# Performance work log

Measured on AMD Instinct MI355X. Metric: run time of the kernel, lower is better.

## Reference

```python
import jax, jax.numpy as jnp
import numpy as np

N_ATOMS = 100000
N_BONDS = 400000
ATOM_FDIM = 133
BOND_FDIM = 147
HIDDEN = 300
DEPTH = 3


def setup_inputs() -> dict:
    key = jax.random.key(0)
    ks = jax.random.split(key, 10)
    f_atoms = jax.random.normal(ks[0], (N_ATOMS, ATOM_FDIM), dtype=jnp.float32)
    f_bonds = jax.random.normal(ks[1], (N_BONDS, BOND_FDIM), dtype=jnp.float32)
    b2a = jax.random.randint(ks[2], (N_BONDS,), 0, N_ATOMS)
    b2revb = jax.random.randint(ks[3], (N_BONDS,), 0, N_BONDS)
    s_i = 1.0 / np.sqrt(BOND_FDIM)
    s_h = 1.0 / np.sqrt(HIDDEN)
    s_o = 1.0 / np.sqrt(ATOM_FDIM + HIDDEN)
    Wi_w = jax.random.uniform(ks[4], (HIDDEN, BOND_FDIM), jnp.float32, -s_i, s_i)
    Wi_b = jax.random.uniform(ks[5], (HIDDEN,), jnp.float32, -s_i, s_i)
    Wh_w = jax.random.uniform(ks[6], (HIDDEN, HIDDEN), jnp.float32, -s_h, s_h)
    Wh_b = jax.random.uniform(ks[7], (HIDDEN,), jnp.float32, -s_h, s_h)
    Wo_w = jax.random.uniform(ks[8], (HIDDEN, ATOM_FDIM + HIDDEN), jnp.float32, -s_o, s_o)
    Wo_b = jax.random.uniform(ks[9], (HIDDEN,), jnp.float32, -s_o, s_o)
    return {"f_atoms": f_atoms, "f_bonds": f_bonds, "b2a": b2a, "b2revb": b2revb,
            "Wi_w": Wi_w, "Wi_b": Wi_b, "Wh_w": Wh_w, "Wh_b": Wh_b,
            "Wo_w": Wo_w, "Wo_b": Wo_b}


def reference(f_atoms, f_bonds, b2a, b2revb, Wi_w, Wi_b, Wh_w, Wh_b, Wo_w, Wo_b):
    n_atoms = f_atoms.shape[0]
    # initial bond messages: [n_bonds, hidden]
    H_bonds = jax.nn.relu(f_bonds @ Wi_w.T + Wi_b)
    dest = b2a[b2revb]  # destination atom of each directed bond
    for _ in range(DEPTH - 1):
        # scatter-add bond messages onto destination atoms
        sum_msgs = jax.ops.segment_sum(H_bonds, dest, num_segments=n_atoms)
        # gather back to bonds from source atoms, subtract reverse-bond message
        msgs = sum_msgs[b2a] - H_bonds[b2revb]
        H_bonds = jax.nn.relu(H_bonds + msgs @ Wh_w.T + Wh_b)
    sum_msgs = jax.ops.segment_sum(H_bonds, dest, num_segments=n_atoms)
    H_atoms = jax.nn.relu(jnp.concatenate([f_atoms, sum_msgs], axis=1) @ Wo_w.T + Wo_b)
    return (H_atoms, H_bonds)
```

## Files before the change

kernel.cpp:

```cpp
#include <hip/hip_runtime.h>
#include <hip/hip_bf16.h>

#define NB 400000
#define NA 100000
#define AFD 133
#define BFD 147
#define HID 300
#define NP  320
#define SMP 304
#define NT  98

typedef short short8 __attribute__((ext_vector_type(8)));
typedef float f32x4 __attribute__((ext_vector_type(4)));

__device__ __forceinline__ ushort f2b(float f) {
    union { float f; unsigned u; } v; v.f = f;
    unsigned r = v.u + 0x7fffu + ((v.u >> 16) & 1u);
    return (ushort)(r >> 16);
}
__device__ __forceinline__ float b2f(ushort u) {
    union { unsigned u; float f; } v; v.u = ((unsigned)u) << 16;
    return v.f;
}

#define GLDS(gp, lp) __builtin_amdgcn_global_load_lds( \
    (const __attribute__((address_space(1))) void*)(gp), \
    (__attribute__((address_space(3))) void*)(lp), 16, 0, 0)


__global__ void pad_w_k(const float* __restrict__ W, ushort* __restrict__ Wp,
                        int N, int K, int Kp) {
    int idx = blockIdx.x * 256 + threadIdx.x;
    if (idx >= NP * Kp) return;
    int n = idx / Kp, k = idx - n * Kp;
    int t = k >> 5, kk = k & 31;
    int g = kk >> 3, s = kk & 7;
    int gp = g ^ ((n >> 1) & 3);
    ushort v = (n < N && k < K) ? f2b(W[n * K + k]) : (ushort)0;
    Wp[(size_t)t * 10240 + n * 32 + gp * 8 + s] = v;
}

__global__ void pad_bias_k(const float* __restrict__ bh, float* __restrict__ bhp) {
    int i = blockIdx.x * 256 + threadIdx.x;
    if (i < NP) bhp[i] = (i < HID) ? bh[i] : 0.f;
}

__global__ void dest_k(const int* __restrict__ b2a, const int* __restrict__ b2revb,
                       int* __restrict__ dest) {
    int b = blockIdx.x * 256 + threadIdx.x;
    if (b < NB) dest[b] = b2a[b2revb[b]];
}

__global__ void count_k(const int* __restrict__ dest, int* __restrict__ cnt) {
    int b = blockIdx.x * 256 + threadIdx.x;
    if (b < NB) atomicAdd(&cnt[dest[b]], 1);
}

__global__ void scanA_k(const int* __restrict__ cnt, int* __restrict__ tsum) {
    __shared__ int sm[256];
    const int tid = threadIdx.x;
    int base = blockIdx.x * 1024 + tid * 4;
    int s = 0;
#pragma unroll
    for (int j = 0; j < 4; ++j) { int i = base + j; if (i < NA) s += cnt[i]; }
    sm[tid] = s; __syncthreads();
    for (int o = 128; o > 0; o >>= 1) {
        if (tid < o) sm[tid] += sm[tid + o];
        __syncthreads();
    }
    if (tid == 0) tsum[blockIdx.x] = sm[0];
}

__global__ void scanB_k(const int* __restrict__ tsum, int* __restrict__ toff,
                        int* __restrict__ rs) {
    if (threadIdx.x == 0) {
        int run = 0;
        for (int t = 0; t < NT; ++t) { toff[t] = run; run += tsum[t]; }
        rs[NA] = run;
    }
}

__global__ void scanC_k(const int* __restrict__ cnt, const int* __restrict__ toff,
                        int* __restrict__ rs) {
    __shared__ int sm[256];
    const int tid = threadIdx.x;
    int base = blockIdx.x * 1024 + tid * 4;
    int v[4]; int s = 0;
#pragma unroll
    for (int j = 0; j < 4; ++j) {
        v[j] = (base + j < NA) ? cnt[base + j] : 0;
        s += v[j];
    }
    sm[tid] = s; __syncthreads();
    for (int o = 1; o < 256; o <<= 1) {
        int x = (tid >= o) ? sm[tid - o] : 0;
        __syncthreads();
        sm[tid] += x;
        __syncthreads();
    }
    int acc = sm[tid] - s + toff[blockIdx.x];
#pragma unroll
    for (int j = 0; j < 4; ++j) {
        if (base + j < NA) rs[base + j] = acc;
        acc += v[j];
    }
}

__global__ void scatter_k(const int* __restrict__ dest, const int* __restrict__ rs,
                          int* __restrict__ cur, int* __restrict__ bl) {
    int b = blockIdx.x * 256 + threadIdx.x;
    if (b >= NB) return;
    int a = dest[b];
    int pos = rs[a] + atomicAdd(&cur[a], 1);
    bl[pos] = b;
}

template<int MODE>
__global__ __launch_bounds__(512) void gemm_k(
    const float* __restrict__ F1, const float* __restrict__ Sum,
    const ushort* __restrict__ W, const float* __restrict__ bias,
    ushort* __restrict__ Cb, float* __restrict__ Cf, int M)
{
    constexpr int KP = (MODE == 0) ? 192 : 448;
    constexpr int TILES = KP / 32;
    static_assert(KP % 64 == 0 && TILES % 2 == 0, "XOR swizzle needs 128B rows, even tiles");
    __shared__ ushort As[128 * KP];
    __shared__ ushort Bs[2][320 * 32];

    const int tid = threadIdx.x;
    const int w = tid >> 6, lane = tid & 63;
    const int wr = w >> 2, wc = w & 3;
    const int g = lane >> 4, lr = lane & 15;
    const int m0 = blockIdx.x * 128;

    {
        const int row = tid >> 2, q = tid & 3;
        int grow = m0 + row;
        if (MODE == 2 && grow >= M) grow = M - 1;
        const int axw = (row & 7) << 4;
        char* abase = (char*)As + (size_t)row * (KP * 2);
#pragma unroll
        for (int t = 0; t < TILES; ++t) {
            const int k0 = t * 32 + q * 8;
            ushort o[8];
            if (MODE == 0) {
                const float* src = F1 + (size_t)grow * BFD;
#pragma unroll
                for (int s = 0; s < 8; ++s)
                    o[s] = (k0 + s < BFD) ? f2b(src[k0 + s]) : (ushort)0;
            } else {
#pragma unroll
                for (int s = 0; s < 8; ++s) {
                    int k = k0 + s;
                    float x = 0.f;
                    if (k < AFD) x = F1[(size_t)grow * AFD + k];
                    else if (k < AFD + SMP) x = Sum[(size_t)grow * SMP + (k - AFD)];
                    o[s] = f2b(x);
                }
            }
            ushort* dst = (ushort*)(abase + ((t * 64 + q * 16) ^ axw));
            *(ushort4*)dst       = make_ushort4(o[0], o[1], o[2], o[3]);
            *(ushort4*)(dst + 4) = make_ushort4(o[4], o[5], o[6], o[7]);
        }
    }

    auto stageB = [&](int t, int buf) {
        const ushort* wt = W + (size_t)t * 10240;
        ushort* bs = &Bs[buf][0];
        GLDS(wt + (size_t)w * 512 + lane * 8,        bs + w * 512);
        GLDS(wt + (size_t)(w + 8) * 512 + lane * 8,  bs + (w + 8) * 512);
        if (w < 4)
            GLDS(wt + (size_t)(w + 16) * 512 + lane * 8, bs + (w + 16) * 512);
    };

    f32x4 acc[4][5];
#pragma unroll
    for (int mi = 0; mi < 4; ++mi)
#pragma unroll
        for (int ni = 0; ni < 5; ++ni) acc[mi][ni] = (f32x4){0.f, 0.f, 0.f, 0.f};

    stageB(0, 0);
    __syncthreads();

    const int raxw = (lr & 7) << 4;
    const int bswz = (lr >> 1) & 3;
    for (int t = 0; t < TILES; ++t) {
        if (t + 1 < TILES) stageB(t + 1, (t + 1) & 1);
        const ushort* bs = &Bs[t & 1][0];
        short8 af[4];
#pragma unroll
        for (int mi = 0; mi < 4; ++mi) {
            const int r = wr * 64 + mi * 16 + lr;
            af[mi] = *(const short8*)((const char*)As + (size_t)r * (KP * 2)
                                      + ((t * 64 + g * 16) ^ raxw));
        }
#pragma unroll
        for (int ni = 0; ni < 5; ++ni) {
            const int c = wc * 80 + ni * 16 + lr;
            short8 bf = *(const short8*)&bs[c * 32 + ((g ^ bswz) << 3)];
#pragma unroll
            for (int mi = 0; mi < 4; ++mi)
                acc[mi][ni] = __builtin_amdgcn_mfma_f32_16x16x32_bf16(af[mi], bf, acc[mi][ni], 0, 0, 0);
        }
        __syncthreads();
    }

#pragma unroll
    for (int ni = 0; ni < 5; ++ni) {
        const int col = wc * 80 + ni * 16 + lr;
        const float bv = (col < HID) ? bias[col] : 0.f;
#pragma unroll
        for (int mi = 0; mi < 4; ++mi) {
            const int row0 = m0 + wr * 64 + mi * 16 + g * 4;
#pragma unroll
            for (int r = 0; r < 4; ++r) {
                const int row = row0 + r;
                float v = fmaxf(acc[mi][ni][r] + bv, 0.f);
                if (MODE == 2) {
                    if (col < HID && row < M) Cf[(size_t)row * HID + col] = v;
                } else {
                    Cb[(size_t)row * NP + col] = f2b(v);
                }
            }
        }
    }
}

__global__ __launch_bounds__(512) void gemm_h_k(
    const ushort* __restrict__ Hb, const ushort* __restrict__ W,
    ushort* __restrict__ Y)
{
    __shared__ ushort As[2][4][128][8];
    __shared__ ushort Bs[2][320 * 32];
    const int tid = threadIdx.x;
    const int w = tid >> 6, lane = tid & 63;
    const int wr = w >> 2, wc = w & 3;
    const int g = lane >> 4, lr = lane & 15;
    const int m0 = blockIdx.x * 128;

    const int q = w >> 1, r0 = (w & 1) * 64;
    const ushort* aglob = Hb + (size_t)(m0 + r0 + lane) * NP + q * 8;

    f32x4 acc[4][5];
#pragma unroll
    for (int mi = 0; mi < 4; ++mi)
#pragma unroll
        for (int ni = 0; ni < 5; ++ni) acc[mi][ni] = (f32x4){0.f, 0.f, 0.f, 0.f};

    auto stageA = [&](int t, int buf) {
        GLDS(aglob + t * 32, &As[buf][q][r0][0]);
    };
    auto stageB = [&](int t, int buf) {
        const ushort* wt = W + (size_t)t * 10240;
        ushort* bs = &Bs[buf][0];
        GLDS(wt + (size_t)w * 512 + lane * 8,        bs + w * 512);
        GLDS(wt + (size_t)(w + 8) * 512 + lane * 8,  bs + (w + 8) * 512);
        if (w < 4)
            GLDS(wt + (size_t)(w + 16) * 512 + lane * 8, bs + (w + 16) * 512);
    };

    stageA(0, 0); stageB(0, 0);
    __syncthreads();

    const int bswz = (lr >> 1) & 3;
    for (int t = 0; t < 10; ++t) {
        if (t < 9) { stageA(t + 1, (t + 1) & 1); stageB(t + 1, (t + 1) & 1); }
        const int buf = t & 1;
        short8 af[4];
#pragma unroll
        for (int mi = 0; mi < 4; ++mi)
            af[mi] = *(const short8*)&As[buf][g][wr * 64 + mi * 16 + lr][0];
#pragma unroll
        for (int ni = 0; ni < 5; ++ni) {
            const int c = wc * 80 + ni * 16 + lr;
            short8 bf = *(const short8*)&Bs[buf][c * 32 + ((g ^ bswz) << 3)];
#pragma unroll
            for (int mi = 0; mi < 4; ++mi)
                acc[mi][ni] = __builtin_amdgcn_mfma_f32_16x16x32_bf16(af[mi], bf, acc[mi][ni], 0, 0, 0);
        }
        __syncthreads();
    }

#pragma unroll
    for (int ni = 0; ni < 5; ++ni) {
        const int col = wc * 80 + ni * 16 + lr;
#pragma unroll
        for (int mi = 0; mi < 4; ++mi) {
            const int row0 = m0 + wr * 64 + mi * 16 + g * 4;
#pragma unroll
            for (int r = 0; r < 4; ++r)
                Y[(size_t)(row0 + r) * NP + col] = f2b(acc[mi][ni][r]);
        }
    }
}

__global__ void seg_sum_bf16_k(const ushort* __restrict__ Y, const int* __restrict__ rs,
                               const int* __restrict__ bl, ushort* __restrict__ SY) {
    int idx = blockIdx.x * 256 + threadIdx.x;
    if (idx >= NA * 40) return;
    int a = idx / 40, c = (idx - a * 40) * 8;
    int s0 = rs[a], s1 = rs[a + 1];
    float acc[8] = {0.f, 0.f, 0.f, 0.f, 0.f, 0.f, 0.f, 0.f};
    for (int j = s0; j < s1; ++j) {
        const ushort* p = &Y[(size_t)bl[j] * NP + c];
        ushort4 u0 = *(const ushort4*)p, u1 = *(const ushort4*)(p + 4);
        acc[0] += b2f(u0.x); acc[1] += b2f(u0.y);
        acc[2] += b2f(u0.z); acc[3] += b2f(u0.w);
        acc[4] += b2f(u1.x); acc[5] += b2f(u1.y);
        acc[6] += b2f(u1.z); acc[7] += b2f(u1.w);
    }
    ushort* dst = &SY[(size_t)a * NP + c];
    *(ushort4*)dst       = make_ushort4(f2b(acc[0]), f2b(acc[1]), f2b(acc[2]), f2b(acc[3]));
    *(ushort4*)(dst + 4) = make_ushort4(f2b(acc[4]), f2b(acc[5]), f2b(acc[6]), f2b(acc[7]));
}

template<bool OUTF>
__global__ void update_k(ushort* __restrict__ Hb, const ushort* __restrict__ SY,
                         const ushort* __restrict__ Y,
                         const int* __restrict__ b2a, const int* __restrict__ b2revb,
                         const float* __restrict__ bhp, float* __restrict__ Hbonds) {
    int idx = blockIdx.x * 256 + threadIdx.x;
    if (idx >= NB * 40) return;
    int b = idx / 40, c = (idx - b * 40) * 8;
    int sa = b2a[b], rb = b2revb[b];
    ushort* hp = &Hb[(size_t)b * NP + c];
    const ushort* sp = &SY[(size_t)sa * NP + c];
    const ushort* yp = &Y[(size_t)rb * NP + c];
    ushort4 h0 = *(const ushort4*)hp,       h1 = *(const ushort4*)(hp + 4);
    ushort4 s0 = *(const ushort4*)sp,       s1 = *(const ushort4*)(sp + 4);
    ushort4 y0 = *(const ushort4*)yp,       y1 = *(const ushort4*)(yp + 4);
    float4 bl0 = *(const float4*)&bhp[c], bl1 = *(const float4*)&bhp[c + 4];
    float v[8];
    v[0] = fmaxf(b2f(h0.x) + b2f(s0.x) - b2f(y0.x) + bl0.x, 0.f);
    v[1] = fmaxf(b2f(h0.y) + b2f(s0.y) - b2f(y0.y) + bl0.y, 0.f);
    v[2] = fmaxf(b2f(h0.z) + b2f(s0.z) - b2f(y0.z) + bl0.z, 0.f);
    v[3] = fmaxf(b2f(h0.w) + b2f(s0.w) - b2f(y0.w) + bl0.w, 0.f);
    v[4] = fmaxf(b2f(h1.x) + b2f(s1.x) - b2f(y1.x) + bl1.x, 0.f);
    v[5] = fmaxf(b2f(h1.y) + b2f(s1.y) - b2f(y1.y) + bl1.y, 0.f);
    v[6] = fmaxf(b2f(h1.z) + b2f(s1.z) - b2f(y1.z) + bl1.z, 0.f);
    v[7] = fmaxf(b2f(h1.w) + b2f(s1.w) - b2f(y1.w) + bl1.w, 0.f);
    *(ushort4*)hp       = make_ushort4(f2b(v[0]), f2b(v[1]), f2b(v[2]), f2b(v[3]));
    *(ushort4*)(hp + 4) = make_ushort4(f2b(v[4]), f2b(v[5]), f2b(v[6]), f2b(v[7]));
    if (OUTF && c < HID) {
        float* op = &Hbonds[(size_t)b * HID + c];
        *(float4*)op = make_float4(v[0], v[1], v[2], v[3]);
        if (c + 4 < HID) *(float4*)(op + 4) = make_float4(v[4], v[5], v[6], v[7]);
    }
}

__global__ void seg_sum_csr_k(const ushort* __restrict__ Hb, const int* __restrict__ rs,
                              const int* __restrict__ bl, float* __restrict__ sum) {
    int idx = blockIdx.x * 256 + threadIdx.x;
    if (idx >= NA * 38) return;
    int a = idx / 38, c = (idx - a * 38) * 8;
    int s0 = rs[a], s1 = rs[a + 1];
    float acc[8] = {0.f, 0.f, 0.f, 0.f, 0.f, 0.f, 0.f, 0.f};
    for (int j = s0; j < s1; ++j) {
        const ushort* p = &Hb[(size_t)bl[j] * NP + c];
        ushort4 u0 = *(const ushort4*)p, u1 = *(const ushort4*)(p + 4);
        acc[0] += b2f(u0.x); acc[1] += b2f(u0.y);
        acc[2] += b2f(u0.z); acc[3] += b2f(u0.w);
        acc[4] += b2f(u1.x); acc[5] += b2f(u1.y);
        acc[6] += b2f(u1.z); acc[7] += b2f(u1.w);
    }
    float* dst = &sum[(size_t)a * SMP + c];
    *(float4*)dst       = make_float4(acc[0], acc[1], acc[2], acc[3]);
    *(float4*)(dst + 4) = make_float4(acc[4], acc[5], acc[6], acc[7]);
}

extern "C" void kernel_launch(void* const* d_in, const int* in_sizes, int n_in,
                              void* d_out, int out_size, void* d_ws, size_t ws_size,
                              hipStream_t stream) {
    const float* f_atoms = (const float*)d_in[0];
    const float* f_bonds = (const float*)d_in[1];
    const int*   b2a     = (const int*)d_in[2];
    const int*   b2revb  = (const int*)d_in[3];
    const float* Wi_w    = (const float*)d_in[4];
    const float* Wi_b    = (const float*)d_in[5];
    const float* Wh_w    = (const float*)d_in[6];
    const float* Wh_b    = (const float*)d_in[7];
    const float* Wo_w    = (const float*)d_in[8];
    const float* Wo_b    = (const float*)d_in[9];
    float* out = (float*)d_out;

    char* ws = (char*)d_ws;
    ushort* Hb   = (ushort*)ws;            ws += (size_t)NB * NP * 2;
    ushort* Y    = (ushort*)ws;            ws += (size_t)NB * NP * 2;
    ushort* SY   = (ushort*)ws;            ws += (size_t)NA * NP * 2;
    float*  sum  = (float*)ws;             ws += (size_t)NA * SMP * 4;
    int*    dest = (int*)ws;               ws += (size_t)NB * 4;
    ushort* Wp0  = (ushort*)ws;            ws += (size_t)6  * 10240 * 2;
    ushort* Wp1  = (ushort*)ws;            ws += (size_t)10 * 10240 * 2;
    ushort* Wp2  = (ushort*)ws;            ws += (size_t)14 * 10240 * 2;
    float*  bhp  = (float*)ws;             ws += (size_t)NP * 4;
    int*    cnt  = (int*)ws;               ws += (size_t)NA * 4;
    int*    cur  = (int*)ws;               ws += (size_t)NA * 4;
    int*    rs   = (int*)ws;               ws += (size_t)(NA + 1) * 4;
    int*    bl   = (int*)ws;               ws += (size_t)NB * 4;
    int*    tsum = (int*)ws;               ws += 128 * 4;
    int*    toff = (int*)ws;               ws += 128 * 4;
    float* Hatoms = out;
    float* Hbonds = out + (size_t)NA * HID;

    pad_w_k<<<(NP * 192 + 255) / 256, 256, 0, stream>>>(Wi_w, Wp0, HID, BFD, 192);
    pad_w_k<<<(NP * NP  + 255) / 256, 256, 0, stream>>>(Wh_w, Wp1, HID, HID, NP);
    pad_w_k<<<(NP * 448 + 255) / 256, 256, 0, stream>>>(Wo_w, Wp2, HID, AFD + HID, 448);
    pad_bias_k<<<2, 256, 0, stream>>>(Wh_b, bhp);
    dest_k<<<(NB + 255) / 256, 256, 0, stream>>>(b2a, b2revb, dest);
    hipMemsetAsync(cnt, 0, (size_t)NA * 4, stream);
    hipMemsetAsync(cur, 0, (size_t)NA * 4, stream);
    count_k<<<(NB + 255) / 256, 256, 0, stream>>>(dest, cnt);
    scanA_k<<<NT, 256, 0, stream>>>(cnt, tsum);
    scanB_k<<<1, 64, 0, stream>>>(tsum, toff, rs);
    scanC_k<<<NT, 256, 0, stream>>>(cnt, toff, rs);
    scatter_k<<<(NB + 255) / 256, 256, 0, stream>>>(dest, rs, cur, bl);

    gemm_k<0><<<NB / 128, 512, 0, stream>>>(
        f_bonds, nullptr, Wp0, Wi_b, Hb, nullptr, NB);

    for (int it = 0; it < 2; ++it) {
        gemm_h_k<<<NB / 128, 512, 0, stream>>>(Hb, Wp1, Y);
        seg_sum_bf16_k<<<(NA * 40 + 255) / 256, 256, 0, stream>>>(Y, rs, bl, SY);
        if (it == 0)
            update_k<false><<<(NB * 40 + 255) / 256, 256, 0, stream>>>(
                Hb, SY, Y, b2a, b2revb, bhp, nullptr);
        else
            update_k<true><<<(NB * 40 + 255) / 256, 256, 0, stream>>>(
                Hb, SY, Y, b2a, b2revb, bhp, Hbonds);
    }

    seg_sum_csr_k<<<(NA * 38 + 255) / 256, 256, 0, stream>>>(Hb, rs, bl, sum);
    gemm_k<2><<<(NA + 127) / 128, 512, 0, stream>>>(
        f_atoms, sum, Wp2, Wo_b, nullptr, Hatoms, NA);
}
```

Measured before the change: 1.538 ms.

## Reorder message passing: aggregate before GEMM and fuse update into GEMM epilogue

Uses linearity, sum[b2a]W − H[rev]W, to move the segment-sum ahead of the Wh matmul. Bond states are aggregated to atoms first, a small atom-sized GEMM follows, and the bond GEMM reads rows gathered by b2revb. The residual/bias/ReLU update now runs in that GEMM's epilogue, reading H and the gathered atom result directly. This removes the full bond-sized Y intermediate and the separate update kernel, at the cost of an extra atom GEMM, gathered A-tile loads, and scalar epilogue loads. Bond buffers are ping-ponged so the epilogue never reads rows it has already overwritten.

```diff
diff --git a/kernel.cpp b/kernel.cpp
--- a/kernel.cpp
+++ b/kernel.cpp
@@ -226,9 +226,9 @@
     }
 }
 
-__global__ __launch_bounds__(512) void gemm_h_k(
-    const ushort* __restrict__ Hb, const ushort* __restrict__ W,
-    ushort* __restrict__ Y)
+__global__ __launch_bounds__(512) void gemm_a_k(
+    const ushort* __restrict__ A, const ushort* __restrict__ W,
+    ushort* __restrict__ C, int M)
 {
     __shared__ ushort As[2][4][128][8];
     __shared__ ushort Bs[2][320 * 32];
@@ -239,7 +239,8 @@
     const int m0 = blockIdx.x * 128;
 
     const int q = w >> 1, r0 = (w & 1) * 64;
-    const ushort* aglob = Hb + (size_t)(m0 + r0 + lane) * NP + q * 8;
+    int srow = m0 + r0 + lane; if (srow >= M) srow = M - 1;
+    const ushort* aglob = A + (size_t)srow * NP + q * 8;
 
     f32x4 acc[4][5];
 #pragma unroll
@@ -247,9 +248,7 @@
 #pragma unroll
         for (int ni = 0; ni < 5; ++ni) acc[mi][ni] = (f32x4){0.f, 0.f, 0.f, 0.f};
 
-    auto stageA = [&](int t, int buf) {
-        GLDS(aglob + t * 32, &As[buf][q][r0][0]);
-    };
+    auto stageA = [&](int t, int buf) { GLDS(aglob + t * 32, &As[buf][q][r0][0]); };
     auto stageB = [&](int t, int buf) {
         const ushort* wt = W + (size_t)t * 10240;
         ushort* bs = &Bs[buf][0];
@@ -289,63 +288,109 @@
             const int row0 = m0 + wr * 64 + mi * 16 + g * 4;
 #pragma unroll
             for (int r = 0; r < 4; ++r)
-                Y[(size_t)(row0 + r) * NP + col] = f2b(acc[mi][ni][r]);
-        }
-    }
-}
-
-__global__ void seg_sum_bf16_k(const ushort* __restrict__ Y, const int* __restrict__ rs,
-                               const int* __restrict__ bl, ushort* __restrict__ SY) {
+                if (row0 + r < M) C[(size_t)(row0 + r) * NP + col] = f2b(acc[mi][ni][r]);
+        }
+    }
+}
+
+template<bool OUTF>
+__global__ __launch_bounds__(512) void gemm_u_k(
+    const ushort* __restrict__ HbIn, const ushort* __restrict__ W,
+    const ushort* __restrict__ SYa,
+    const int* __restrict__ b2a, const int* __restrict__ b2revb,
+    const float* __restrict__ bhp,
+    ushort* __restrict__ HbOut, float* __restrict__ Hbonds)
+{
+    __shared__ ushort As[2][4][128][8];
+    __shared__ ushort Bs[2][320 * 32];
+    const int tid = threadIdx.x;
+    const int w = tid >> 6, lane = tid & 63;
+    const int wr = w >> 2, wc = w & 3;
+    const int g = lane >> 4, lr = lane & 15;
+    const int m0 = blockIdx.x * 128;
+
+    const int q = w >> 1, r0 = (w & 1) * 64;
+    const int rrow = b2revb[m0 + r0 + lane];
+    const ushort* aglob = HbIn + (size_t)rrow * NP + q * 8;
+
+    f32x4 acc[4][5];
+#pragma unroll
+    for (int mi = 0; mi < 4; ++mi)
+#pragma unroll
+        for (int ni = 0; ni < 5; ++ni) acc[mi][ni] = (f32x4){0.f, 0.f, 0.f, 0.f};
+
+    auto stageA = [&](int t, int buf) { GLDS(aglob + t * 32, &As[buf][q][r0][0]); };
+    auto stageB = [&](int t, int buf) {
+        const ushort* wt = W + (size_t)t * 10240;
+        ushort* bs = &Bs[buf][0];
+        GLDS(wt + (size_t)w * 512 + lane * 8,        bs + w * 512);
+        GLDS(wt + (size_t)(w + 8) * 512 + lane * 8,  bs + (w + 8) * 512);
+        if (w < 4)
+            GLDS(wt + (size_t)(w + 16) * 512 + lane * 8, bs + (w + 16) * 512);
+    };
+
+    stageA(0, 0); stageB(0, 0);
+    __syncthreads();
+
+    const int bswz = (lr >> 1) & 3;
+    for (int t = 0; t < 10; ++t) {
+        if (t < 9) { stageA(t + 1, (t + 1) & 1); stageB(t + 1, (t + 1) & 1); }
+        const int buf = t & 1;
+        short8 af[4];
+#pragma unroll
+        for (int mi = 0; mi < 4; ++mi)
+            af[mi] = *(const short8*)&As[buf][g][wr * 64 + mi * 16 + lr][0];
+#pragma unroll
+        for (int ni = 0; ni < 5; ++ni) {
+            const int c = wc * 80 + ni * 16 + lr;
+            short8 bf = *(const short8*)&Bs[buf][c * 32 + ((g ^ bswz) << 3)];
+#pragma unroll
+            for (int mi = 0; mi < 4; ++mi)
+                acc[mi][ni] = __builtin_amdgcn_mfma_f32_16x16x32_bf16(af[mi], bf, acc[mi][ni], 0, 0, 0);
+        }
+        __syncthreads();
+    }
+
+    float bv[5];
+#pragma unroll
+    for (int ni = 0; ni < 5; ++ni) bv[ni] = bhp[wc * 80 + ni * 16 + lr];
+#pragma unroll
+    for (int mi = 0; mi < 4; ++mi) {
+#pragma unroll
+        for (int r = 0; r < 4; ++r) {
+            const int row = m0 + wr * 64 + mi * 16 + g * 4 + r;
+            const int sa = b2a[row];
+            const ushort* hp = &HbIn[(size_t)row * NP];
+            const ushort* sp = &SYa[(size_t)sa * NP];
+#pragma unroll
+            for (int ni = 0; ni < 5; ++ni) {
+                const int col = wc * 80 + ni * 16 + lr;
+                float v = fmaxf(b2f(hp[col]) + b2f(sp[col]) - acc[mi][ni][r] + bv[ni], 0.f);
+                HbOut[(size_t)row * NP + col] = f2b(v);
+                if (OUTF && col < HID) Hbonds[(size_t)row * HID + col] = v;
+            }
+        }
+    }
+}
+
+__global__ void seg_sum_bf16_k(const ushort* __restrict__ H, const int* __restrict__ rs,
+                               const int* __restrict__ bl, ushort* __restrict__ SH) {
     int idx = blockIdx.x * 256 + threadIdx.x;
     if (idx >= NA * 40) return;
     int a = idx / 40, c = (idx - a * 40) * 8;
     int s0 = rs[a], s1 = rs[a + 1];
     float acc[8] = {0.f, 0.f, 0.f, 0.f, 0.f, 0.f, 0.f, 0.f};
     for (int j = s0; j < s1; ++j) {
-        const ushort* p = &Y[(size_t)bl[j] * NP + c];
+        const ushort* p = &H[(size_t)bl[j] * NP + c];
         ushort4 u0 = *(const ushort4*)p, u1 = *(const ushort4*)(p + 4);
         acc[0] += b2f(u0.x); acc[1] += b2f(u0.y);
         acc[2] += b2f(u0.z); acc[3] += b2f(u0.w);
         acc[4] += b2f(u1.x); acc[5] += b2f(u1.y);
         acc[6] += b2f(u1.z); acc[7] += b2f(u1.w);
     }
-    ushort* dst = &SY[(size_t)a * NP + c];
+    ushort* dst = &SH[(size_t)a * NP + c];
     *(ushort4*)dst       = make_ushort4(f2b(acc[0]), f2b(acc[1]), f2b(acc[2]), f2b(acc[3]));
     *(ushort4*)(dst + 4) = make_ushort4(f2b(acc[4]), f2b(acc[5]), f2b(acc[6]), f2b(acc[7]));
-}
-
-template<bool OUTF>
-__global__ void update_k(ushort* __restrict__ Hb, const ushort* __restrict__ SY,
-                         const ushort* __restrict__ Y,
-                         const int* __restrict__ b2a, const int* __restrict__ b2revb,
-                         const float* __restrict__ bhp, float* __restrict__ Hbonds) {
-    int idx = blockIdx.x * 256 + threadIdx.x;
-    if (idx >= NB * 40) return;
-    int b = idx / 40, c = (idx - b * 40) * 8;
-    int sa = b2a[b], rb = b2revb[b];
-    ushort* hp = &Hb[(size_t)b * NP + c];
-    const ushort* sp = &SY[(size_t)sa * NP + c];
-    const ushort* yp = &Y[(size_t)rb * NP + c];
-    ushort4 h0 = *(const ushort4*)hp,       h1 = *(const ushort4*)(hp + 4);
-    ushort4 s0 = *(const ushort4*)sp,       s1 = *(const ushort4*)(sp + 4);
-    ushort4 y0 = *(const ushort4*)yp,       y1 = *(const ushort4*)(yp + 4);
-    float4 bl0 = *(const float4*)&bhp[c], bl1 = *(const float4*)&bhp[c + 4];
-    float v[8];
-    v[0] = fmaxf(b2f(h0.x) + b2f(s0.x) - b2f(y0.x) + bl0.x, 0.f);
-    v[1] = fmaxf(b2f(h0.y) + b2f(s0.y) - b2f(y0.y) + bl0.y, 0.f);
-    v[2] = fmaxf(b2f(h0.z) + b2f(s0.z) - b2f(y0.z) + bl0.z, 0.f);
-    v[3] = fmaxf(b2f(h0.w) + b2f(s0.w) - b2f(y0.w) + bl0.w, 0.f);
-    v[4] = fmaxf(b2f(h1.x) + b2f(s1.x) - b2f(y1.x) + bl1.x, 0.f);
-    v[5] = fmaxf(b2f(h1.y) + b2f(s1.y) - b2f(y1.y) + bl1.y, 0.f);
-    v[6] = fmaxf(b2f(h1.z) + b2f(s1.z) - b2f(y1.z) + bl1.z, 0.f);
-    v[7] = fmaxf(b2f(h1.w) + b2f(s1.w) - b2f(y1.w) + bl1.w, 0.f);
-    *(ushort4*)hp       = make_ushort4(f2b(v[0]), f2b(v[1]), f2b(v[2]), f2b(v[3]));
-    *(ushort4*)(hp + 4) = make_ushort4(f2b(v[4]), f2b(v[5]), f2b(v[6]), f2b(v[7]));
-    if (OUTF && c < HID) {
-        float* op = &Hbonds[(size_t)b * HID + c];
-        *(float4*)op = make_float4(v[0], v[1], v[2], v[3]);
-        if (c + 4 < HID) *(float4*)(op + 4) = make_float4(v[4], v[5], v[6], v[7]);
-    }
 }
 
 __global__ void seg_sum_csr_k(const ushort* __restrict__ Hb, const int* __restrict__ rs,
@@ -384,9 +429,10 @@
     float* out = (float*)d_out;
 
     char* ws = (char*)d_ws;
-    ushort* Hb   = (ushort*)ws;            ws += (size_t)NB * NP * 2;
-    ushort* Y    = (ushort*)ws;            ws += (size_t)NB * NP * 2;
-    ushort* SY   = (ushort*)ws;            ws += (size_t)NA * NP * 2;
+    ushort* Hb0  = (ushort*)ws;            ws += (size_t)NB * NP * 2;
+    ushort* Hb1  = (ushort*)ws;            ws += (size_t)NB * NP * 2;
+    ushort* SHb  = (ushort*)ws;            ws += (size_t)NA * NP * 2;
+    ushort* SYa  = (ushort*)ws;            ws += (size_t)NA * NP * 2;
     float*  sum  = (float*)ws;             ws += (size_t)NA * SMP * 4;
     int*    dest = (int*)ws;               ws += (size_t)NB * 4;
     ushort* Wp0  = (ushort*)ws;            ws += (size_t)6  * 10240 * 2;
@@ -416,20 +462,19 @@
     scatter_k<<<(NB + 255) / 256, 256, 0, stream>>>(dest, rs, cur, bl);
 
     gemm_k<0><<<NB / 128, 512, 0, stream>>>(
-        f_bonds, nullptr, Wp0, Wi_b, Hb, nullptr, NB);
-
-    for (int it = 0; it < 2; ++it) {
-        gemm_h_k<<<NB / 128, 512, 0, stream>>>(Hb, Wp1, Y);
-        seg_sum_bf16_k<<<(NA * 40 + 255) / 256, 256, 0, stream>>>(Y, rs, bl, SY);
-        if (it == 0)
-            update_k<false><<<(NB * 40 + 255) / 256, 256, 0, stream>>>(
-                Hb, SY, Y, b2a, b2revb, bhp, nullptr);
-        else
-            update_k<true><<<(NB * 40 + 255) / 256, 256, 0, stream>>>(
-                Hb, SY, Y, b2a, b2revb, bhp, Hbonds);
-    }
-
-    seg_sum_csr_k<<<(NA * 38 + 255) / 256, 256, 0, stream>>>(Hb, rs, bl, sum);
+        f_bonds, nullptr, Wp0, Wi_b, Hb0, nullptr, NB);
+
+    seg_sum_bf16_k<<<(NA * 40 + 255) / 256, 256, 0, stream>>>(Hb0, rs, bl, SHb);
+    gemm_a_k<<<(NA + 127) / 128, 512, 0, stream>>>(SHb, Wp1, SYa, NA);
+    gemm_u_k<false><<<NB / 128, 512, 0, stream>>>(
+        Hb0, Wp1, SYa, b2a, b2revb, bhp, Hb1, nullptr);
+
+    seg_sum_bf16_k<<<(NA * 40 + 255) / 256, 256, 0, stream>>>(Hb1, rs, bl, SHb);
+    gemm_a_k<<<(NA + 127) / 128, 512, 0, stream>>>(SHb, Wp1, SYa, NA);
+    gemm_u_k<true><<<NB / 128, 512, 0, stream>>>(
+        Hb1, Wp1, SYa, b2a, b2revb, bhp, Hb0, Hbonds);
+
+    seg_sum_csr_k<<<(NA * 38 + 255) / 256, 256, 0, stream>>>(Hb0, rs, bl, sum);
     gemm_k<2><<<(NA + 127) / 128, 512, 0, stream>>>(
         f_atoms, sum, Wp2, Wo_b, nullptr, Hatoms, NA);
 }
```

Result: slower. 1.680 ms (+9.2%).
